# Performance work log

Measured on AMD Instinct MI355X. Metric: run time of the kernel, lower is better.

Reference implementation:

```python
import jax, jax.numpy as jnp
import numpy as np

N_NODES, D, B, NEG2, DRUG_NUM = 20000, 512, 2048, 64, 2000
H1, H2 = 128, 64


def setup_inputs() -> dict:
    ks = jax.random.split(jax.random.key(0), 10)
    embed = jax.random.normal(ks[0], (N_NODES, D), dtype=jnp.float32)
    h = jax.random.randint(ks[1], (B, 1), 0, DRUG_NUM)
    t = jax.random.randint(ks[2], (B, 1), 0, N_NODES)
    n_s = jax.random.randint(ks[3], (B, NEG2), 0, DRUG_NUM)  # all < drug_num -> chunk branch
    s1 = 1.0 / np.sqrt(2 * D)
    s2 = 1.0 / np.sqrt(H1)
    s3 = 1.0 / np.sqrt(H2)
    W1 = jax.random.uniform(ks[4], (2 * D, H1), minval=-s1, maxval=s1, dtype=jnp.float32)
    b1 = jax.random.uniform(ks[5], (H1,), minval=-s1, maxval=s1, dtype=jnp.float32)
    W2 = jax.random.uniform(ks[6], (H1, H2), minval=-s2, maxval=s2, dtype=jnp.float32)
    b2 = jax.random.uniform(ks[7], (H2,), minval=-s2, maxval=s2, dtype=jnp.float32)
    W3 = jax.random.uniform(ks[8], (H2, 1), minval=-s3, maxval=s3, dtype=jnp.float32)
    b3 = jax.random.uniform(ks[9], (1,), minval=-s3, maxval=s3, dtype=jnp.float32)
    return {"embed": embed, "W1": W1, "b1": b1, "W2": W2, "b2": b2, "W3": W3, "b3": b3,
            "h": h, "t": t, "n_s": n_s}


def _mlp(x, W1, b1, W2, b2, W3, b3):
    # [..., 2D] -> [...] score
    x = jax.nn.relu(x @ W1 + b1)
    x = jax.nn.relu(x @ W2 + b2)
    return (x @ W3 + b3)[..., 0]


def reference(embed, W1, b1, W2, b2, W3, b3, h, t, n_s):
    K = n_s.shape[1] // 2
    n_t, n_h = n_s[:, :K], n_s[:, K:]
    h_e = embed[h]          # [B, 1, D]
    t_e = embed[t]          # [B, T, D]
    T = t.shape[1]
    # positive pairs: [B, T]
    pos = _mlp(jnp.concatenate([jnp.tile(h_e, (1, T, 1)), t_e], axis=-1),
               W1, b1, W2, b2, W3, b3)
    # corrupted-tail negatives: [B, K]
    neg1 = _mlp(jnp.concatenate([jnp.tile(h_e, (1, K, 1)), embed[n_t]], axis=-1),
                W1, b1, W2, b2, W3, b3)
    # corrupted-head negatives: [B, T*K] (T=1 here)
    neg2 = _mlp(jnp.concatenate([embed[n_h], jnp.tile(t_e, (1, K, 1))], axis=-1),
                W1, b1, W2, b2, W3, b3)
    neg = jnp.concatenate([neg1, neg2], axis=1)  # [B, 2K]
    return pos, neg
```

## Files before the change

### kernel.cpp

```cpp
#include <hip/hip_runtime.h>

#define NNODES 20000
#define DIM    512
#define BATCH  2048
#define NDRUG  2000
#define H1     128
#define H2     64
#define NITEM  65
#define DQ     256
#define SLAB   774144

typedef __attribute__((ext_vector_type(8))) short short8;
typedef __attribute__((ext_vector_type(4))) float floatx4;

__device__ inline unsigned short f2bf(float x) {
    union { float f; unsigned u; } v; v.f = x;
    unsigned r = v.u + 0x7fffu + ((v.u >> 16) & 1u);
    return (unsigned short)(r >> 16);
}

__global__ void prep_w2(const float* __restrict__ W2, float* __restrict__ ws)
{
    short8* dst = (short8*)(ws + 2 * (size_t)SLAB);
    const int lane = threadIdx.x & 63;
    const int n = lane & 15, q = lane >> 4;
    #pragma unroll
    for (int kt = 0; kt < 4; ++kt) {
        #pragma unroll
        for (int nt = 0; nt < 4; ++nt) {
            short8 v;
            #pragma unroll
            for (int j = 0; j < 8; ++j) {
                int k = kt * 32 + q * 8 + j;
                v[j] = (short)f2bf(W2[k * H2 + nt * 16 + n]);
            }
            dst[(kt * 4 + nt) * 64 + lane] = v;
        }
    }
}

__global__ __launch_bounds__(512) void layer1_partial(
    const float* __restrict__ embed, const float* __restrict__ W1,
    const int* __restrict__ t, float* __restrict__ ws)
{
    __shared__ float lds_e[16 * DQ];
    const int s   = blockIdx.y;
    const int blk = blockIdx.x;
    const bool isPQ = blk < 125;
    const int rowbase = isPQ ? blk * 16 : (blk - 125) * 16;
    const int o  = threadIdx.x & 127;
    const int rg = threadIdx.x >> 7;
    const int d0 = s * DQ;

    #pragma unroll
    for (int i = 0; i < 2; ++i) {
        int idx = i * 512 + threadIdx.x;
        int r = idx >> 6, c4 = idx & 63;
        int grow = isPQ ? (rowbase + r) : t[rowbase + r];
        *(float4*)(lds_e + r * DQ + c4 * 4) =
            *(const float4*)(embed + (size_t)grow * DIM + d0 + c4 * 4);
    }
    __syncthreads();

    float* Pp  = ws + (size_t)s * SLAB;
    float* Qp  = Pp + NDRUG * H1;
    float* Qtp = Qp + NDRUG * H1;

    if (isPQ) {
        float accT[4] = {0.f,0.f,0.f,0.f}, accB[4] = {0.f,0.f,0.f,0.f};
        float wT[4], wB[4];
        #pragma unroll
        for (int e = 0; e < 4; ++e) {
            wT[e] = W1[(d0 + e) * H1 + o];
            wB[e] = W1[(DIM + d0 + e) * H1 + o];
        }
        for (int d = 0; d < DQ; d += 4) {
            const int dn = (d + 4 < DQ) ? d + 4 : d;
            float nT[4], nB[4];
            #pragma unroll
            for (int e = 0; e < 4; ++e) {
                nT[e] = W1[(d0 + dn + e) * H1 + o];
                nB[e] = W1[(DIM + d0 + dn + e) * H1 + o];
            }
            #pragma unroll
            for (int r = 0; r < 4; ++r) {
                float4 ev = *(const float4*)(lds_e + (rg * 4 + r) * DQ + d);
                accT[r] = fmaf(ev.x, wT[0], accT[r]);
                accT[r] = fmaf(ev.y, wT[1], accT[r]);
                accT[r] = fmaf(ev.z, wT[2], accT[r]);
                accT[r] = fmaf(ev.w, wT[3], accT[r]);
                accB[r] = fmaf(ev.x, wB[0], accB[r]);
                accB[r] = fmaf(ev.y, wB[1], accB[r]);
                accB[r] = fmaf(ev.z, wB[2], accB[r]);
                accB[r] = fmaf(ev.w, wB[3], accB[r]);
            }
            #pragma unroll
            for (int e = 0; e < 4; ++e) { wT[e] = nT[e]; wB[e] = nB[e]; }
        }
        #pragma unroll
        for (int r = 0; r < 4; ++r) {
            int row = rowbase + rg * 4 + r;
            Pp[(size_t)row * H1 + o] = accT[r];
            Qp[(size_t)row * H1 + o] = accB[r];
        }
    } else {
        float accB[4] = {0.f,0.f,0.f,0.f};
        float wB[4];
        #pragma unroll
        for (int e = 0; e < 4; ++e) wB[e] = W1[(DIM + d0 + e) * H1 + o];
        for (int d = 0; d < DQ; d += 4) {
            const int dn = (d + 4 < DQ) ? d + 4 : d;
            float nB[4];
            #pragma unroll
            for (int e = 0; e < 4; ++e) nB[e] = W1[(DIM + d0 + dn + e) * H1 + o];
            #pragma unroll
            for (int r = 0; r < 4; ++r) {
                float4 ev = *(const float4*)(lds_e + (rg * 4 + r) * DQ + d);
                accB[r] = fmaf(ev.x, wB[0], accB[r]);
                accB[r] = fmaf(ev.y, wB[1], accB[r]);
                accB[r] = fmaf(ev.z, wB[2], accB[r]);
                accB[r] = fmaf(ev.w, wB[3], accB[r]);
            }
            #pragma unroll
            for (int e = 0; e < 4; ++e) wB[e] = nB[e];
        }
        #pragma unroll
        for (int r = 0; r < 4; ++r) {
            int row = rowbase + rg * 4 + r;
            Qtp[(size_t)row * H1 + o] = accB[r];
        }
    }
}

__global__ __launch_bounds__(256) void reduce_kernel(float* __restrict__ ws)
{
    int i = (blockIdx.x * 256 + threadIdx.x) * 8;
    float4 a0 = *(const float4*)(ws + i);
    float4 a1 = *(const float4*)(ws + i + 4);
    float4 b0 = *(const float4*)(ws + SLAB + i);
    float4 b1v = *(const float4*)(ws + SLAB + i + 4);
    a0.x += b0.x; a0.y += b0.y; a0.z += b0.z; a0.w += b0.w;
    a1.x += b1v.x; a1.y += b1v.y; a1.z += b1v.z; a1.w += b1v.w;
    *(float4*)(ws + i)     = a0;
    *(float4*)(ws + i + 4) = a1;
}

__global__ __launch_bounds__(256) void score_mfma(
    const float* __restrict__ ws,
    const float* __restrict__ b1, const float* __restrict__ b2,
    const float* __restrict__ W3, const float* __restrict__ b3,
    const int* __restrict__ h, const int* __restrict__ ns,
    float* __restrict__ out)
{
    const float* P  = ws;
    const float* Q  = ws + NDRUG * H1;
    const float* Qt = Q + NDRUG * H1;
    const short8* W2f = (const short8*)(ws + 2 * (size_t)SLAB);

    const int lane = threadIdx.x & 63;
    const int wv   = threadIdx.x >> 6;
    const int tile = blockIdx.x * 4 + wv;
    const int n = lane & 15, q = lane >> 4;

    const int sg   = tile * 16 + n;
    const int b    = sg / NITEM;
    const int item = sg - b * NITEM;
    const float *Pr, *Qr;
    if (item == 0)       { Pr = P + h[b] * H1;                      Qr = Qt + b * H1; }
    else if (item <= 32) { Pr = P + h[b] * H1;                      Qr = Q + ns[b * 64 + item - 1] * H1; }
    else                 { Pr = P + ns[b * 64 + 32 + item - 33] * H1; Qr = Qt + b * H1; }

    floatx4 acc[4];
    #pragma unroll
    for (int nt = 0; nt < 4; ++nt) acc[nt] = (floatx4){0.f, 0.f, 0.f, 0.f};

    #pragma unroll
    for (int kt = 0; kt < 4; ++kt) {
        const int kb = kt * 32 + q * 8;
        float4 p0 = *(const float4*)(Pr + kb);
        float4 p1 = *(const float4*)(Pr + kb + 4);
        float4 q0 = *(const float4*)(Qr + kb);
        float4 q1 = *(const float4*)(Qr + kb + 4);
        float4 c0 = *(const float4*)(b1 + kb);
        float4 c1 = *(const float4*)(b1 + kb + 4);
        short8 af;
        af[0] = (short)f2bf(fmaxf(p0.x + q0.x + c0.x, 0.f));
        af[1] = (short)f2bf(fmaxf(p0.y + q0.y + c0.y, 0.f));
        af[2] = (short)f2bf(fmaxf(p0.z + q0.z + c0.z, 0.f));
        af[3] = (short)f2bf(fmaxf(p0.w + q0.w + c0.w, 0.f));
        af[4] = (short)f2bf(fmaxf(p1.x + q1.x + c1.x, 0.f));
        af[5] = (short)f2bf(fmaxf(p1.y + q1.y + c1.y, 0.f));
        af[6] = (short)f2bf(fmaxf(p1.z + q1.z + c1.z, 0.f));
        af[7] = (short)f2bf(fmaxf(p1.w + q1.w + c1.w, 0.f));
        #pragma unroll
        for (int nt = 0; nt < 4; ++nt) {
            short8 bf = W2f[(kt * 4 + nt) * 64 + lane];
            acc[nt] = __builtin_amdgcn_mfma_f32_16x16x32_bf16(af, bf, acc[nt], 0, 0, 0);
        }
    }

    float part[4];
    #pragma unroll
    for (int reg = 0; reg < 4; ++reg) {
        float sum = 0.f;
        #pragma unroll
        for (int nt = 0; nt < 4; ++nt) {
            int j = nt * 16 + n;
            sum = fmaf(fmaxf(acc[nt][reg] + b2[j], 0.f), W3[j], sum);
        }
        part[reg] = sum;
    }
    #pragma unroll
    for (int m = 1; m < 16; m <<= 1) {
        #pragma unroll
        for (int reg = 0; reg < 4; ++reg)
            part[reg] += __shfl_xor(part[reg], m, 64);
    }
    if (n == 0) {
        const float base3 = b3[0];
        #pragma unroll
        for (int reg = 0; reg < 4; ++reg) {
            int gid = tile * 16 + q * 4 + reg;
            int bb  = gid / NITEM;
            int it  = gid - bb * NITEM;
            float val = part[reg] + base3;
            if (it == 0) out[bb] = val;
            else         out[BATCH + bb * 64 + (it - 1)] = val;
        }
    }
}

extern "C" void kernel_launch(void* const* d_in, const int* in_sizes, int n_in,
                              void* d_out, int out_size, void* d_ws, size_t ws_size,
                              hipStream_t stream) {
    const float* embed = (const float*)d_in[0];
    const float* W1    = (const float*)d_in[1];
    const float* b1    = (const float*)d_in[2];
    const float* W2    = (const float*)d_in[3];
    const float* b2    = (const float*)d_in[4];
    const float* W3    = (const float*)d_in[5];
    const float* b3    = (const float*)d_in[6];
    const int*   h     = (const int*)d_in[7];
    const int*   t     = (const int*)d_in[8];
    const int*   ns    = (const int*)d_in[9];
    float* out = (float*)d_out;
    float* ws  = (float*)d_ws;

    prep_w2<<<1, 64, 0, stream>>>(W2, ws);

    dim3 grid1(253, 2);
    layer1_partial<<<grid1, 512, 0, stream>>>(embed, W1, t, ws);
    reduce_kernel<<<SLAB / (256 * 8), 256, 0, stream>>>(ws);

    score_mfma<<<(BATCH * NITEM) / 64, 256, 0, stream>>>(ws, b1, b2, W3, b3,
                                                         h, ns, out);
}
```

Before: 139.2 us.

## Compute layer-1 projections with bf16 MFMA and 4-way split-K

Replaces the scalar fp32 FMA layer-1 projection kernel with a bf16 MFMA kernel. A new prep kernel converts the drug embeddings, the gathered tail embeddings, W1 and W2 into bf16 fragment layouts in the workspace. K is split four ways across waves, and a four-slab reduce sums the partials. The aim is to move the dominant layer-1 GEMM onto matrix cores, at the cost of bf16 rounding of the layer-1 inputs, an extra conversion pass, and more workspace traffic.

```diff
diff --git a/kernel.cpp b/kernel.cpp
--- a/kernel.cpp
+++ b/kernel.cpp
@@ -1,14 +1,16 @@
 #include <hip/hip_runtime.h>
 
-#define NNODES 20000
 #define DIM    512
 #define BATCH  2048
 #define NDRUG  2000
 #define H1     128
 #define H2     64
 #define NITEM  65
-#define DQ     256
 #define SLAB   774144
+#define W2F_OFF (4 * SLAB)
+#define W1F_OFF (W2F_OFF + 4096)
+#define X1_OFF  (W1F_OFF + 65536)
+#define X2_OFF  (X1_OFF + 512000)
 
 typedef __attribute__((ext_vector_type(8))) short short8;
 typedef __attribute__((ext_vector_type(4))) float floatx4;
@@ -19,130 +21,135 @@
     return (unsigned short)(r >> 16);
 }
 
-__global__ void prep_w2(const float* __restrict__ W2, float* __restrict__ ws)
-{
-    short8* dst = (short8*)(ws + 2 * (size_t)SLAB);
-    const int lane = threadIdx.x & 63;
-    const int n = lane & 15, q = lane >> 4;
-    #pragma unroll
-    for (int kt = 0; kt < 4; ++kt) {
-        #pragma unroll
-        for (int nt = 0; nt < 4; ++nt) {
+__device__ inline short8 cvt8(const float* __restrict__ src) {
+    float4 a = *(const float4*)src, b = *(const float4*)(src + 4);
+    short8 v;
+    v[0] = (short)f2bf(a.x); v[1] = (short)f2bf(a.y);
+    v[2] = (short)f2bf(a.z); v[3] = (short)f2bf(a.w);
+    v[4] = (short)f2bf(b.x); v[5] = (short)f2bf(b.y);
+    v[6] = (short)f2bf(b.z); v[7] = (short)f2bf(b.w);
+    return v;
+}
+
+__global__ __launch_bounds__(256) void prep(
+    const float* __restrict__ embed, const float* __restrict__ W1,
+    const float* __restrict__ W2, const int* __restrict__ t,
+    float* __restrict__ ws)
+{
+    const int blk = blockIdx.x, tid = threadIdx.x;
+    if (blk < 125) {
+        short8* X1 = (short8*)(ws + X1_OFF);
+        #pragma unroll
+        for (int i = 0; i < 4; ++i) {
+            int u = blk * 1024 + i * 256 + tid;
+            int row = u >> 6, c = u & 63;
+            X1[u] = cvt8(embed + (size_t)row * DIM + c * 8);
+        }
+    } else if (blk < 253) {
+        short8* X2 = (short8*)(ws + X2_OFF);
+        #pragma unroll
+        for (int i = 0; i < 4; ++i) {
+            int u = (blk - 125) * 1024 + i * 256 + tid;
+            int row = u >> 6, c = u & 63;
+            X2[u] = cvt8(embed + (size_t)t[row] * DIM + c * 8);
+        }
+    } else if (blk < 255) {
+        short8* W1f = (short8*)(ws + W1F_OFF);
+        #pragma unroll
+        for (int i = 0; i < 32; ++i) {
+            int item = (blk - 253) * 8192 + i * 256 + tid;
+            int frag = item >> 6, lane = item & 63;
+            int half = frag >> 7, ktot = (frag >> 3) & 15, nt = frag & 7;
+            int n = lane & 15, q = lane >> 4;
             short8 v;
             #pragma unroll
             for (int j = 0; j < 8; ++j) {
-                int k = kt * 32 + q * 8 + j;
-                v[j] = (short)f2bf(W2[k * H2 + nt * 16 + n]);
+                int k = half * DIM + ktot * 32 + q * 8 + j;
+                v[j] = (short)f2bf(W1[k * H1 + nt * 16 + n]);
             }
-            dst[(kt * 4 + nt) * 64 + lane] = v;
-        }
-    }
-}
-
-__global__ __launch_bounds__(512) void layer1_partial(
-    const float* __restrict__ embed, const float* __restrict__ W1,
-    const int* __restrict__ t, float* __restrict__ ws)
-{
-    __shared__ float lds_e[16 * DQ];
-    const int s   = blockIdx.y;
-    const int blk = blockIdx.x;
-    const bool isPQ = blk < 125;
-    const int rowbase = isPQ ? blk * 16 : (blk - 125) * 16;
-    const int o  = threadIdx.x & 127;
-    const int rg = threadIdx.x >> 7;
-    const int d0 = s * DQ;
-
-    #pragma unroll
-    for (int i = 0; i < 2; ++i) {
-        int idx = i * 512 + threadIdx.x;
-        int r = idx >> 6, c4 = idx & 63;
-        int grow = isPQ ? (rowbase + r) : t[rowbase + r];
-        *(float4*)(lds_e + r * DQ + c4 * 4) =
-            *(const float4*)(embed + (size_t)grow * DIM + d0 + c4 * 4);
-    }
-    __syncthreads();
-
-    float* Pp  = ws + (size_t)s * SLAB;
-    float* Qp  = Pp + NDRUG * H1;
-    float* Qtp = Qp + NDRUG * H1;
-
-    if (isPQ) {
-        float accT[4] = {0.f,0.f,0.f,0.f}, accB[4] = {0.f,0.f,0.f,0.f};
-        float wT[4], wB[4];
-        #pragma unroll
-        for (int e = 0; e < 4; ++e) {
-            wT[e] = W1[(d0 + e) * H1 + o];
-            wB[e] = W1[(DIM + d0 + e) * H1 + o];
-        }
-        for (int d = 0; d < DQ; d += 4) {
-            const int dn = (d + 4 < DQ) ? d + 4 : d;
-            float nT[4], nB[4];
+            W1f[item] = v;
+        }
+    } else {
+        short8* W2f = (short8*)(ws + W2F_OFF);
+        #pragma unroll
+        for (int i = 0; i < 4; ++i) {
+            int item = i * 256 + tid;
+            int frag = item >> 6, lane = item & 63;
+            int kt = frag >> 2, nt = frag & 3;
+            int n = lane & 15, q = lane >> 4;
+            short8 v;
             #pragma unroll
-            for (int e = 0; e < 4; ++e) {
-                nT[e] = W1[(d0 + dn + e) * H1 + o];
-                nB[e] = W1[(DIM + d0 + dn + e) * H1 + o];
-            }
-            #pragma unroll
-            for (int r = 0; r < 4; ++r) {
-                float4 ev = *(const float4*)(lds_e + (rg * 4 + r) * DQ + d);
-                accT[r] = fmaf(ev.x, wT[0], accT[r]);
-                accT[r] = fmaf(ev.y, wT[1], accT[r]);
-                accT[r] = fmaf(ev.z, wT[2], accT[r]);
-                accT[r] = fmaf(ev.w, wT[3], accT[r]);
-                accB[r] = fmaf(ev.x, wB[0], accB[r]);
-                accB[r] = fmaf(ev.y, wB[1], accB[r]);
-                accB[r] = fmaf(ev.z, wB[2], accB[r]);
-                accB[r] = fmaf(ev.w, wB[3], accB[r]);
-            }
-            #pragma unroll
-            for (int e = 0; e < 4; ++e) { wT[e] = nT[e]; wB[e] = nB[e]; }
-        }
-        #pragma unroll
-        for (int r = 0; r < 4; ++r) {
-            int row = rowbase + rg * 4 + r;
-            Pp[(size_t)row * H1 + o] = accT[r];
-            Qp[(size_t)row * H1 + o] = accB[r];
-        }
+            for (int j = 0; j < 8; ++j)
+                v[j] = (short)f2bf(W2[(kt * 32 + q * 8 + j) * H2 + nt * 16 + n]);
+            W2f[item] = v;
+        }
+    }
+}
+
+__global__ __launch_bounds__(256) void layer1_mfma(float* __restrict__ ws)
+{
+    const short8* W1f = (const short8*)(ws + W1F_OFF);
+    const int lane = threadIdx.x & 63;
+    const int w    = blockIdx.x * 4 + (threadIdx.x >> 6);
+    const int n = lane & 15, q = lane >> 4;
+
+    const short8* Xrow;
+    float* obase;
+    int half, ntsel, kc;
+    if (w < 2000) {
+        int rt = w >> 4, rem = w & 15, cg = rem >> 2;
+        kc = rem & 3;
+        Xrow = (const short8*)(ws + X1_OFF) + (size_t)(rt * 16 + n) * 64 + kc * 16;
+        half  = cg >> 1;
+        ntsel = (cg & 1) * 4;
+        obase = ws + (size_t)kc * SLAB + half * (NDRUG * H1)
+                   + (size_t)(rt * 16) * H1 + (cg & 1) * 64;
     } else {
-        float accB[4] = {0.f,0.f,0.f,0.f};
-        float wB[4];
-        #pragma unroll
-        for (int e = 0; e < 4; ++e) wB[e] = W1[(DIM + d0 + e) * H1 + o];
-        for (int d = 0; d < DQ; d += 4) {
-            const int dn = (d + 4 < DQ) ? d + 4 : d;
-            float nB[4];
-            #pragma unroll
-            for (int e = 0; e < 4; ++e) nB[e] = W1[(DIM + d0 + dn + e) * H1 + o];
-            #pragma unroll
-            for (int r = 0; r < 4; ++r) {
-                float4 ev = *(const float4*)(lds_e + (rg * 4 + r) * DQ + d);
-                accB[r] = fmaf(ev.x, wB[0], accB[r]);
-                accB[r] = fmaf(ev.y, wB[1], accB[r]);
-                accB[r] = fmaf(ev.z, wB[2], accB[r]);
-                accB[r] = fmaf(ev.w, wB[3], accB[r]);
-            }
-            #pragma unroll
-            for (int e = 0; e < 4; ++e) wB[e] = nB[e];
-        }
-        #pragma unroll
-        for (int r = 0; r < 4; ++r) {
-            int row = rowbase + rg * 4 + r;
-            Qtp[(size_t)row * H1 + o] = accB[r];
-        }
-    }
-}
-
-__global__ __launch_bounds__(256) void reduce_kernel(float* __restrict__ ws)
+        int w2 = w - 2000;
+        int rt = w2 >> 3, rem = w2 & 7, cg = rem >> 2;
+        kc = rem & 3;
+        Xrow = (const short8*)(ws + X2_OFF) + (size_t)(rt * 16 + n) * 64 + kc * 16;
+        half  = 1;
+        ntsel = cg * 4;
+        obase = ws + (size_t)kc * SLAB + 2 * (NDRUG * H1)
+                   + (size_t)(rt * 16) * H1 + cg * 64;
+    }
+
+    floatx4 acc[4];
+    #pragma unroll
+    for (int nt = 0; nt < 4; ++nt) acc[nt] = (floatx4){0.f, 0.f, 0.f, 0.f};
+
+    #pragma unroll
+    for (int kt = 0; kt < 4; ++kt) {
+        short8 af = Xrow[kt * 4 + q];
+        #pragma unroll
+        for (int nt = 0; nt < 4; ++nt) {
+            short8 bf = W1f[(size_t)((half * 16 + kc * 4 + kt) * 8 + ntsel + nt) * 64 + lane];
+            acc[nt] = __builtin_amdgcn_mfma_f32_16x16x32_bf16(af, bf, acc[nt], 0, 0, 0);
+        }
+    }
+
+    #pragma unroll
+    for (int nt = 0; nt < 4; ++nt)
+        #pragma unroll
+        for (int reg = 0; reg < 4; ++reg)
+            obase[(q * 4 + reg) * H1 + nt * 16 + n] = acc[nt][reg];
+}
+
+__global__ __launch_bounds__(256) void reduce4(float* __restrict__ ws)
 {
     int i = (blockIdx.x * 256 + threadIdx.x) * 8;
-    float4 a0 = *(const float4*)(ws + i);
-    float4 a1 = *(const float4*)(ws + i + 4);
-    float4 b0 = *(const float4*)(ws + SLAB + i);
-    float4 b1v = *(const float4*)(ws + SLAB + i + 4);
-    a0.x += b0.x; a0.y += b0.y; a0.z += b0.z; a0.w += b0.w;
-    a1.x += b1v.x; a1.y += b1v.y; a1.z += b1v.z; a1.w += b1v.w;
-    *(float4*)(ws + i)     = a0;
-    *(float4*)(ws + i + 4) = a1;
+    #pragma unroll
+    for (int half = 0; half < 2; ++half) {
+        int o = i + half * 4;
+        float4 a = *(const float4*)(ws + o);
+        float4 b = *(const float4*)(ws + SLAB + o);
+        float4 c = *(const float4*)(ws + 2 * SLAB + o);
+        float4 d = *(const float4*)(ws + 3 * SLAB + o);
+        a.x += b.x + c.x + d.x;  a.y += b.y + c.y + d.y;
+        a.z += b.z + c.z + d.z;  a.w += b.w + c.w + d.w;
+        *(float4*)(ws + o) = a;
+    }
 }
 
 __global__ __launch_bounds__(256) void score_mfma(
@@ -155,7 +162,7 @@
     const float* P  = ws;
     const float* Q  = ws + NDRUG * H1;
     const float* Qt = Q + NDRUG * H1;
-    const short8* W2f = (const short8*)(ws + 2 * (size_t)SLAB);
+    const short8* W2f = (const short8*)(ws + W2F_OFF);
 
     const int lane = threadIdx.x & 63;
     const int wv   = threadIdx.x >> 6;
@@ -166,8 +173,8 @@
     const int b    = sg / NITEM;
     const int item = sg - b * NITEM;
     const float *Pr, *Qr;
-    if (item == 0)       { Pr = P + h[b] * H1;                      Qr = Qt + b * H1; }
-    else if (item <= 32) { Pr = P + h[b] * H1;                      Qr = Q + ns[b * 64 + item - 1] * H1; }
+    if (item == 0)       { Pr = P + h[b] * H1;                        Qr = Qt + b * H1; }
+    else if (item <= 32) { Pr = P + h[b] * H1;                        Qr = Q + ns[b * 64 + item - 1] * H1; }
     else                 { Pr = P + ns[b * 64 + 32 + item - 33] * H1; Qr = Qt + b * H1; }
 
     floatx4 acc[4];
@@ -246,12 +253,9 @@
     float* out = (float*)d_out;
     float* ws  = (float*)d_ws;
 
-    prep_w2<<<1, 64, 0, stream>>>(W2, ws);
-
-    dim3 grid1(253, 2);
-    layer1_partial<<<grid1, 512, 0, stream>>>(embed, W1, t, ws);
-    reduce_kernel<<<SLAB / (256 * 8), 256, 0, stream>>>(ws);
-
+    prep<<<256, 256, 0, stream>>>(embed, W1, W2, t, ws);
+    layer1_mfma<<<756, 256, 0, stream>>>(ws);
+    reduce4<<<SLAB / (256 * 8), 256, 0, stream>>>(ws);
     score_mfma<<<(BATCH * NITEM) / 64, 256, 0, stream>>>(ws, b1, b2, W3, b3,
                                                          h, ns, out);
 }
```

Result: faster. 127.2 us (-8.6%).
